# Optimization experiments

Measured on AMD Instinct MI355X. Metric: run time of the kernel, lower is better.

Reference implementation:

```python
import jax, jax.numpy as jnp
import numpy as np
import math

B, T, M, C, H = 2, 2048, 77, 512, 8
D = C // H  # head dim = 64


def setup_inputs() -> dict:
    key = jax.random.key(0)
    ks = jax.random.split(key, 20)
    s = 0.02
    inp = {
        "x": jax.random.normal(ks[0], (B, T, C), jnp.float32),
        "c": jax.random.normal(ks[1], (B, M, C), jnp.float32),
        # causal mask for self-attention (masked_fill where == 0)
        "attn_mask": jnp.tril(jnp.ones((T, T), jnp.int32))[None, None],
        "padding_mask": jnp.ones((B, M), jnp.int32),
    }
    names = ["Wq", "Wk", "Wv", "Wkc", "Wvc", "Wg1", "Wg2", "Wp"]
    for i, n in enumerate(names):
        inp[n] = jax.random.normal(ks[2 + i], (C, C), jnp.float32) * s
        inp["b" + n[1:]] = jnp.zeros((C,), jnp.float32)
    return inp


def _heads(t):
    # [B, S, C] -> [B, S, H, D]
    return t.reshape(t.shape[0], t.shape[1], H, D)


def reference(x, c, attn_mask, padding_mask,
              Wq, bq, Wk, bk, Wv, bv, Wkc, bkc, Wvc, bvc,
              Wg1, bg1, Wg2, bg2, Wp, bp):
    scale = 1.0 / math.sqrt(D)
    q = _heads(x @ Wq + bq)      # [B,T,H,D]
    k = _heads(x @ Wk + bk)      # [B,T,H,D]
    v = _heads(x @ Wv + bv)
    k_c = _heads(c @ Wkc + bkc)  # [B,M,H,D]
    v_c = _heads(c @ Wvc + bvc)

    # self-attention branch
    att = jnp.einsum("bthd,bshd->bhts", q, k) * scale   # [B,H,T,T]
    att = jnp.where(attn_mask == 0, -jnp.inf, att)
    att = jax.nn.softmax(att, axis=-1)
    y = jnp.einsum("bhts,bshd->bthd", att, v).reshape(B, T, C)

    # cross-attention branch to condition c
    att_c = jnp.einsum("bthd,bmhd->bhtm", q, k_c) * scale  # [B,H,T,M]
    att_c = jnp.where(padding_mask[:, None, None, :] == 0, -jnp.inf, att_c)
    att_c = jax.nn.softmax(att_c, axis=-1)
    y_c = jnp.einsum("bhtm,bmhd->bthd", att_c, v_c).reshape(B, T, C)

    # sigmoid gating fusion (note: gates cross-multiply branches, per source)
    gate_self = jax.nn.sigmoid(y @ Wg1 + bg1)
    gate_c = jax.nn.sigmoid(y_c @ Wg2 + bg2)
    y = gate_self * y_c + gate_c * y
    return y @ Wp + bp
```

## Files before the change

kernel.cpp:

```cpp
#include <hip/hip_runtime.h>
#include <hip/hip_bf16.h>
#include <math.h>

#define BB 2
#define TT 2048
#define MM 77
#define CC 512
#define HH 8
#define DD 64

typedef short bf16x8 __attribute__((ext_vector_type(8)));
typedef float f32x4  __attribute__((ext_vector_type(4)));

static __device__ __forceinline__ unsigned short f2bf(float x) {
    __hip_bfloat16 h = __float2bfloat16(x);
    return *reinterpret_cast<unsigned short*>(&h);
}
static __device__ __forceinline__ float bf2f(unsigned short u) {
    unsigned int v = ((unsigned int)u) << 16;
    return *reinterpret_cast<float*>(&v);
}

__global__ __launch_bounds__(256)
void wconv8(const float* __restrict__ w0, const float* __restrict__ w1,
            const float* __restrict__ w2, const float* __restrict__ w3,
            const float* __restrict__ w4, const float* __restrict__ w5,
            const float* __restrict__ w6, const float* __restrict__ w7,
            unsigned short* __restrict__ outbase,
            const float* __restrict__ x, unsigned short* __restrict__ xb)
{
    const float* W;
    switch (blockIdx.z) {
        case 0: W = w0; break; case 1: W = w1; break;
        case 2: W = w2; break; case 3: W = w3; break;
        case 4: W = w4; break; case 5: W = w5; break;
        case 6: W = w6; break; default: W = w7; break;
    }
    unsigned short* Wp = outbase + (size_t)blockIdx.z * 512 * 512;
    const int k0 = blockIdx.x * 64;
    const int n0 = blockIdx.y * 64;
    const int tid = threadIdx.x;
    __shared__ unsigned short t[64 * 72];

    #pragma unroll
    for (int it = 0; it < 4; ++it) {
        const int e = tid + 256 * it;
        const int r  = e >> 4;
        const int c4 = (e & 15) * 4;
        const float4 v = *(const float4*)(W + (size_t)(k0 + r) * 512 + n0 + c4);
        t[(c4 + 0) * 72 + r] = f2bf(v.x);
        t[(c4 + 1) * 72 + r] = f2bf(v.y);
        t[(c4 + 2) * 72 + r] = f2bf(v.z);
        t[(c4 + 3) * 72 + r] = f2bf(v.w);
    }

    {
        const int lin = (blockIdx.z << 6) + (blockIdx.x << 3) + blockIdx.y;
        const size_t base = (size_t)lin * 8 * 512;
        #pragma unroll
        for (int u = 0; u < 2; ++u) {
            const int unit = tid + 256 * u;
            const float4 a = *(const float4*)(x + base + (size_t)unit * 8);
            const float4 b = *(const float4*)(x + base + (size_t)unit * 8 + 4);
            unsigned short o[8];
            o[0] = f2bf(a.x); o[1] = f2bf(a.y); o[2] = f2bf(a.z); o[3] = f2bf(a.w);
            o[4] = f2bf(b.x); o[5] = f2bf(b.y); o[6] = f2bf(b.z); o[7] = f2bf(b.w);
            *(int4*)(xb + base + (size_t)unit * 8) = *(const int4*)o;
        }
    }

    __syncthreads();
    #pragma unroll
    for (int it = 0; it < 2; ++it) {
        const int e    = tid + 256 * it;
        const int gl   = e >> 7;
        const int ktl  = (e >> 6) & 1;
        const int lane = e & 63;
        const int l15  = lane & 15;
        const int q    = lane >> 4;
        const int4 v = *(const int4*)&t[(gl * 16 + l15) * 72 + ktl * 32 + q * 8];
        const int G  = (n0 >> 4) + gl;
        const int KT = (k0 >> 5) + ktl;
        *(int4*)(Wp + ((size_t)(G * 16 + KT) * 64 + lane) * 8) = v;
    }
}

__global__ __launch_bounds__(256)
void proj_all(const unsigned short* __restrict__ xb, const float* __restrict__ cin,
              const unsigned short* __restrict__ Wt8,
              const float* __restrict__ bq, const float* __restrict__ bk,
              const float* __restrict__ bv, const float* __restrict__ bkc,
              const float* __restrict__ bvc,
              unsigned short* __restrict__ qb,
              unsigned short* __restrict__ vtb,
              unsigned short* __restrict__ kcb,
              unsigned short* __restrict__ vtcb)
{
    __shared__ unsigned short As[2 * 16 * 64 * 8];

    const int tid = threadIdx.x;
    int b = blockIdx.x;
    const unsigned short* Wtp;
    const float *bb0, *bb1, *bb2;
    int row0, colb, N, isSelf;
    float oscale;
    if (b < 768) {
        isSelf = 1;
        row0 = (b & 127) * 32; colb = (b >> 7) * 256;
        Wtp = Wt8; N = BB * TT;
        oscale = 0.125f;
        bb0 = bq; bb1 = bk; bb2 = bv;
    } else {
        b -= 768; isSelf = 0;
        row0 = (b % 5) * 32; colb = (b / 5) * 256;
        Wtp = Wt8 + 3 * 262144; N = BB * MM;
        oscale = 1.0f;
        bb0 = bkc; bb1 = bvc; bb2 = nullptr;
    }

    {
        const int r    = tid >> 3;
        const int rg   = r >> 4;
        const int l15r = r & 15;
        const int seg  = (tid & 7) * 64;
        const int gr   = row0 + r;
        unsigned short tmp[64];
        if (isSelf) {
            #pragma unroll
            for (int jb = 0; jb < 8; ++jb)
                *(int4*)&tmp[jb*8] = *(const int4*)(xb + (size_t)gr * 512 + seg + jb * 8);
        } else {
            #pragma unroll
            for (int j = 0; j < 16; ++j) {
                float4 v = (gr < N) ? *(const float4*)(cin + (size_t)gr * 512 + seg + j * 4)
                                    : make_float4(0.f, 0.f, 0.f, 0.f);
                tmp[j*4+0] = f2bf(v.x); tmp[j*4+1] = f2bf(v.y);
                tmp[j*4+2] = f2bf(v.z); tmp[j*4+3] = f2bf(v.w);
            }
        }
        #pragma unroll
        for (int jb = 0; jb < 8; ++jb) {
            const int k  = seg + jb * 8;
            const int kt = k >> 5;
            const int q  = (k >> 3) & 3;
            *(int4*)&As[((rg * 16 + kt) * 64 + q * 16 + l15r) * 8] = *(int4*)&tmp[jb*8];
        }
    }
    __syncthreads();

    const int wv   = tid >> 6;
    const int lane = tid & 63;
    const int l15  = lane & 15;
    const int quad = lane >> 4;
    const int wc   = colb + wv * 64;
    const int wcg  = wc >> 4;

    f32x4 acc[2][4];
    #pragma unroll
    for (int mi = 0; mi < 2; ++mi)
        #pragma unroll
        for (int ni = 0; ni < 4; ++ni) acc[mi][ni] = (f32x4){0.f, 0.f, 0.f, 0.f};

    bf16x8 b0v[4], b1v[4], b2v[4];
    #pragma unroll
    for (int ni = 0; ni < 4; ++ni) {
        b0v[ni] = *(const bf16x8*)(Wtp + (((size_t)(wcg + ni) * 16 + 0) << 9) + lane * 8);
        b1v[ni] = *(const bf16x8*)(Wtp + (((size_t)(wcg + ni) * 16 + 1) << 9) + lane * 8);
    }

    for (int kt = 0; kt < 16; ++kt) {
        if (kt + 2 < 16) {
            #pragma unroll
            for (int ni = 0; ni < 4; ++ni)
                b2v[ni] = *(const bf16x8*)(Wtp + (((size_t)(wcg + ni) * 16 + kt + 2) << 9) + lane * 8);
        }
        const bf16x8 a0 = *(const bf16x8*)&As[((0 * 16 + kt) * 64 + lane) * 8];
        const bf16x8 a1 = *(const bf16x8*)&As[((1 * 16 + kt) * 64 + lane) * 8];
        #pragma unroll
        for (int ni = 0; ni < 4; ++ni) {
            acc[0][ni] = __builtin_amdgcn_mfma_f32_16x16x32_bf16(a0, b0v[ni], acc[0][ni], 0, 0, 0);
            acc[1][ni] = __builtin_amdgcn_mfma_f32_16x16x32_bf16(a1, b0v[ni], acc[1][ni], 0, 0, 0);
        }
        #pragma unroll
        for (int ni = 0; ni < 4; ++ni) { b0v[ni] = b1v[ni]; b1v[ni] = b2v[ni]; }
    }

    const int which = wc >> 9;
    const float* bsel = (which == 0) ? bb0 : ((which == 1) ? bb1 : bb2);
    const float sc = (which == 0) ? oscale : 1.f;

    float bvv[4];
    #pragma unroll
    for (int ni = 0; ni < 4; ++ni)
        bvv[ni] = bsel[(wc + ni * 16 + l15) & 511];

    if (isSelf) {
        const int b_ = row0 >> 11;
        const int t0 = row0 & 2047;
        const int h  = (wc & 511) >> 6;
        __syncthreads();
        if (which < 2) {
            unsigned short* TL = (unsigned short*)As + wv * (32 * 72);
            #pragma unroll
            for (int mi = 0; mi < 2; ++mi)
                #pragma unroll
                for (int ni = 0; ni < 4; ++ni)
                    #pragma unroll
                    for (int reg = 0; reg < 4; ++reg) {
                        const int t = mi * 16 + quad * 4 + reg;
                        const int d = ni * 16 + l15;
                        TL[t * 72 + d] = f2bf((acc[mi][ni][reg] + bvv[ni]) * sc);
                    }
            unsigned short* dst = qb + (size_t)which * 2097152
                                + (((size_t)b_ * 8 + h) * 2048 + t0) * 64;
            #pragma unroll
            for (int it = 0; it < 4; ++it) {
                const int t = it * 8 + (lane >> 3);
                *(int4*)(dst + (size_t)t * 64 + (lane & 7) * 8)
                    = *(const int4*)&TL[t * 72 + (lane & 7) * 8];
            }
        } else {
            unsigned short* TL = (unsigned short*)As + wv * (64 * 40);
            #pragma unroll
            for (int mi = 0; mi < 2; ++mi)
                #pragma unroll
                for (int ni = 0; ni < 4; ++ni) {
                    ushort4 u;
                    u.x = f2bf(acc[mi][ni][0] + bvv[ni]);
                    u.y = f2bf(acc[mi][ni][1] + bvv[ni]);
                    u.z = f2bf(acc[mi][ni][2] + bvv[ni]);
                    u.w = f2bf(acc[mi][ni][3] + bvv[ni]);
                    const int d = ni * 16 + l15;
                    *(ushort4*)&TL[d * 40 + mi * 16 + quad * 4] = u;
                }
            unsigned short* dst = vtb + (((size_t)b_ * 8 + h) * 64) * 2048 + t0;
            #pragma unroll
            for (int it = 0; it < 4; ++it) {
                const int d = it * 16 + (lane >> 2);
                *(int4*)(dst + (size_t)d * 2048 + (lane & 3) * 8)
                    = *(const int4*)&TL[d * 40 + (lane & 3) * 8];
            }
        }
    } else {
        #pragma unroll
        for (int mi = 0; mi < 2; ++mi)
            #pragma unroll
            for (int reg = 0; reg < 4; ++reg) {
                const int row = row0 + mi * 16 + quad * 4 + reg;
                if (row >= N) continue;
                const int b_ = (row >= MM) ? 1 : 0;
                const int m_ = row - b_ * MM;
                #pragma unroll
                for (int ni = 0; ni < 4; ++ni) {
                    const float v = acc[mi][ni][reg] + bvv[ni];
                    const int cl = (wc + ni * 16 + l15) & 511;
                    const int hh = cl >> 6, d = cl & 63;
                    if (which == 0)
                        kcb[(((size_t)b_ * 8 + hh) * 77 + m_) * 64 + d] = f2bf(v);
                    else
                        vtcb[(((size_t)b_ * 8 + hh) * 64 + d) * 128 + m_] = f2bf(v);
                }
            }
        if (which == 1 && row0 == 0) {
            const int h0 = (colb - 512) >> 6;
            for (int e = tid; e < 2 * 4 * 64; e += 256) {
                const int d  = e & 63;
                const int hl = (e >> 6) & 3;
                const int bz = e >> 8;
                unsigned short* rp = vtcb + (((size_t)bz * 8 + h0 + hl) * 64 + d) * 128;
                rp[77] = 0; rp[78] = 0; rp[79] = 0;
                #pragma unroll
                for (int q8 = 80; q8 < 128; q8 += 8)
                    *(int4*)(rp + q8) = make_int4(0, 0, 0, 0);
            }
        }
    }
}

__global__ __launch_bounds__(256)
void attn_all(const unsigned short* __restrict__ Qh,
              const unsigned short* __restrict__ Kh,
              const unsigned short* __restrict__ Vth,
              unsigned short* __restrict__ yout,
              const unsigned short* __restrict__ Kch,
              const unsigned short* __restrict__ Vtch,
              unsigned short* __restrict__ ycout)
{
    int lin = blockIdx.x;
    int causal, S_kv, W, bh, qt;
    const unsigned short *Kb, *Vb;
    unsigned short* outp;
    if (lin < 512) {
        causal = 1; S_kv = TT; W = TT;
        bh = (lin & 7) | (((lin >> 3) & 1) << 3);
        const int qtr = lin >> 4;
        qt = (qtr < 16) ? (31 - qtr) : (qtr - 16);
        Kb = Kh + (size_t)bh * S_kv * 64;
        Vb = Vth + (size_t)bh * 64 * W;
        outp = yout;
    } else {
        lin -= 512;
        causal = 0; S_kv = MM; W = 128;
        bh = (lin & 7) | (((lin >> 3) & 1) << 3);
        qt = lin >> 4;
        Kb = Kch + (size_t)bh * S_kv * 64;
        Vb = Vtch + (size_t)bh * 64 * W;
        outp = ycout;
    }
    const int n_kt = causal ? (qt + 1) : 2;

    const int tid  = threadIdx.x;
    const int wv   = tid >> 6;
    const int lane = tid & 63;
    const int l15  = lane & 15;
    const int quad = lane >> 4;

    __shared__ unsigned short Ks[64 * 80];
    __shared__ unsigned short Vs[64 * 80];
    __shared__ unsigned short PT[4 * 16 * 72];

    const int t0 = qt * 64 + wv * 16;
    const unsigned short* qptr = Qh + ((size_t)bh * TT + t0 + l15) * 64 + quad * 8;
    const bf16x8 qb0 = *(const bf16x8*)(qptr);
    const bf16x8 qb1 = *(const bf16x8*)(qptr + 32);

    f32x4 Oacc[4];
    #pragma unroll
    for (int dt = 0; dt < 4; ++dt) Oacc[dt] = (f32x4){0.f, 0.f, 0.f, 0.f};
    float l = 0.f;

    int4 kR[2], vR[2];
    {
        #pragma unroll
        for (int it = 0; it < 2; ++it) {
            const int e = tid + 256 * it;
            const int row = e >> 3, blk = e & 7;
            kR[it] = (row < S_kv)
                ? *(const int4*)(Kb + (size_t)row * 64 + blk * 8) : make_int4(0,0,0,0);
            vR[it] = (blk * 8 < W)
                ? *(const int4*)(Vb + (size_t)row * W + blk * 8) : make_int4(0,0,0,0);
        }
        #pragma unroll
        for (int it = 0; it < 2; ++it) {
            const int e = tid + 256 * it;
            const int row = e >> 3, blk = e & 7;
            *(int4*)&Ks[row * 80 + ((blk ^ (row & 7)) * 8)] = kR[it];
            *(int4*)&Vs[row * 80 + ((blk ^ (row & 7)) * 8)] = vR[it];
        }
    }
    __syncthreads();

    for (int kt = 0; kt < n_kt; ++kt) {
        const int s0 = kt * 64;

        if (kt + 1 < n_kt) {
            const int s1 = (kt + 1) * 64;
            #pragma unroll
            for (int it = 0; it < 2; ++it) {
                const int e = tid + 256 * it;
                const int row = e >> 3, blk = e & 7;
                const int s = s1 + row;
                kR[it] = (s < S_kv)
                    ? *(const int4*)(Kb + (size_t)s * 64 + blk * 8) : make_int4(0,0,0,0);
                vR[it] = (s1 + blk * 8 < W)
                    ? *(const int4*)(Vb + (size_t)row * W + s1 + blk * 8) : make_int4(0,0,0,0);
            }
        }

        f32x4 sacc[4];
        __builtin_amdgcn_s_setprio(1);
        #pragma unroll
        for (int mt = 0; mt < 4; ++mt) {
            const int krow = 16 * mt + l15;
            const bf16x8 ka0 = *(const bf16x8*)&Ks[krow * 80 + (((quad    ) ^ (krow & 7)) * 8)];
            const bf16x8 ka1 = *(const bf16x8*)&Ks[krow * 80 + (((quad + 4) ^ (krow & 7)) * 8)];
            sacc[mt] = (f32x4){0.f, 0.f, 0.f, 0.f};
            sacc[mt] = __builtin_amdgcn_mfma_f32_16x16x32_bf16(ka0, qb0, sacc[mt], 0, 0, 0);
            sacc[mt] = __builtin_amdgcn_mfma_f32_16x16x32_bf16(ka1, qb1, sacc[mt], 0, 0, 0);
        }
        __builtin_amdgcn_s_setprio(0);

        float sv[16];
        #pragma unroll
        for (int mt = 0; mt < 4; ++mt)
            #pragma unroll
            for (int reg = 0; reg < 4; ++reg)
                sv[mt * 4 + reg] = sacc[mt][reg];

        const bool cmask = (causal && kt == qt);
        if (cmask || (s0 + 64 > S_kv)) {
            const int lim = cmask ? (t0 + l15) : 0x7fffffff;
            #pragma unroll
            for (int mt = 0; mt < 4; ++mt)
                #pragma unroll
                for (int reg = 0; reg < 4; ++reg) {
                    const int kg = s0 + 16 * mt + quad * 4 + reg;
                    if (kg > lim || kg >= S_kv) sv[mt * 4 + reg] = -INFINITY;
                }
        }

        float p[16], psum = 0.f;
        #pragma unroll
        for (int i = 0; i < 16; ++i) { p[i] = __expf(sv[i]); psum += p[i]; }
        psum += __shfl_xor(psum, 16);
        psum += __shfl_xor(psum, 32);
        l += psum;

        unsigned short* ptw = &PT[wv * 16 * 72 + l15 * 72];
        #pragma unroll
        for (int mt = 0; mt < 4; ++mt) {
            ushort4 u;
            u.x = f2bf(p[mt * 4 + 0]); u.y = f2bf(p[mt * 4 + 1]);
            u.z = f2bf(p[mt * 4 + 2]); u.w = f2bf(p[mt * 4 + 3]);
            *(ushort4*)(ptw + 16 * mt + quad * 4) = u;
        }
        const bf16x8 pb0 = *(const bf16x8*)(ptw + quad * 8);
        const bf16x8 pb1 = *(const bf16x8*)(ptw + quad * 8 + 32);

        __builtin_amdgcn_s_setprio(1);
        #pragma unroll
        for (int dt = 0; dt < 4; ++dt) {
            const int vrow = 16 * dt + l15;
            const bf16x8 va0 = *(const bf16x8*)&Vs[vrow * 80 + (((quad    ) ^ (vrow & 7)) * 8)];
            const bf16x8 va1 = *(const bf16x8*)&Vs[vrow * 80 + (((quad + 4) ^ (vrow & 7)) * 8)];
            Oacc[dt] = __builtin_amdgcn_mfma_f32_16x16x32_bf16(va0, pb0, Oacc[dt], 0, 0, 0);
            Oacc[dt] = __builtin_amdgcn_mfma_f32_16x16x32_bf16(va1, pb1, Oacc[dt], 0, 0, 0);
        }
        __builtin_amdgcn_s_setprio(0);

        if (kt + 1 < n_kt) {
            __syncthreads();
            #pragma unroll
            for (int it = 0; it < 2; ++it) {
                const int e = tid + 256 * it;
                const int row = e >> 3, blk = e & 7;
                *(int4*)&Ks[row * 80 + ((blk ^ (row & 7)) * 8)] = kR[it];
                *(int4*)&Vs[row * 80 + ((blk ^ (row & 7)) * 8)] = vR[it];
            }
            __syncthreads();
        }
    }

    const int b = bh >> 3, h = bh & 7;
    const float inv_l = 1.f / l;
    const int t = t0 + l15;
    unsigned short* ob = outp + ((size_t)b * TT + t) * CC + h * DD + quad * 4;
    #pragma unroll
    for (int dt = 0; dt < 4; ++dt) {
        ushort4 u;
        u.x = f2bf(Oacc[dt][0] * inv_l);
        u.y = f2bf(Oacc[dt][1] * inv_l);
        u.z = f2bf(Oacc[dt][2] * inv_l);
        u.w = f2bf(Oacc[dt][3] * inv_l);
        *(ushort4*)(ob + 16 * dt) = u;
    }
}

__global__ __launch_bounds__(512)
void gates_final(const unsigned short* __restrict__ yb,
                 const unsigned short* __restrict__ ycb,
                 const unsigned short* __restrict__ Wt8,
                 const float* __restrict__ bg1, const float* __restrict__ bg2,
                 const float* __restrict__ bp,
                 float* __restrict__ out)
{
    __shared__ unsigned short Ay[16 * 512];
    __shared__ unsigned short Ac[16 * 512];

    const int tid  = threadIdx.x;
    const int row0 = blockIdx.x * 16;

    {
        const int r  = tid >> 5;
        const int c0 = (tid & 31) * 16;
        const unsigned short* ys = yb  + (size_t)(row0 + r) * 512 + c0;
        const unsigned short* cs = ycb + (size_t)(row0 + r) * 512 + c0;
        #pragma unroll
        for (int jb = 0; jb < 2; ++jb) {
            const int k  = c0 + jb * 8;
            const int kt = k >> 5;
            const int q  = (k >> 3) & 3;
            *(int4*)&Ay[(kt * 64 + q * 16 + r) * 8] = *(const int4*)(ys + jb * 8);
            *(int4*)&Ac[(kt * 64 + q * 16 + r) * 8] = *(const int4*)(cs + jb * 8);
        }
    }
    __syncthreads();

    const int wv   = tid >> 6;
    const int lane = tid & 63;
    const int l15  = lane & 15;
    const int quad = lane >> 4;
    const int wc   = wv * 64;
    const int wcg  = wc >> 4;

    const unsigned short* W1 = Wt8 + 5 * 262144;
    const unsigned short* W2 = Wt8 + 6 * 262144;
    const unsigned short* W3 = Wt8 + 7 * 262144;

    unsigned int g1p[8], g2p[8];

    #pragma unroll
    for (int gg = 0; gg < 2; ++gg) {
        const unsigned short* Wg = gg ? W2 : W1;
        const unsigned short* Ax = gg ? Ac : Ay;
        const float* bg = gg ? bg2 : bg1;
        f32x4 acc[4];
        #pragma unroll
        for (int ni = 0; ni < 4; ++ni) acc[ni] = (f32x4){0.f, 0.f, 0.f, 0.f};
        bf16x8 b0v[4], b1v[4], b2v[4];
        #pragma unroll
        for (int ni = 0; ni < 4; ++ni) {
            b0v[ni] = *(const bf16x8*)(Wg + (((size_t)(wcg + ni) * 16 + 0) << 9) + lane * 8);
            b1v[ni] = *(const bf16x8*)(Wg + (((size_t)(wcg + ni) * 16 + 1) << 9) + lane * 8);
        }
        for (int kt = 0; kt < 16; ++kt) {
            if (kt + 2 < 16) {
                #pragma unroll
                for (int ni = 0; ni < 4; ++ni)
                    b2v[ni] = *(const bf16x8*)(Wg + (((size_t)(wcg + ni) * 16 + kt + 2) << 9) + lane * 8);
            }
            const bf16x8 a = *(const bf16x8*)&Ax[(kt * 64 + lane) * 8];
            #pragma unroll
            for (int ni = 0; ni < 4; ++ni)
                acc[ni] = __builtin_amdgcn_mfma_f32_16x16x32_bf16(a, b0v[ni], acc[ni], 0, 0, 0);
            #pragma unroll
            for (int ni = 0; ni < 4; ++ni) { b0v[ni] = b1v[ni]; b1v[ni] = b2v[ni]; }
        }
        #pragma unroll
        for (int ni = 0; ni < 4; ++ni) {
            const float bv = bg[wc + ni * 16 + l15];
            float s[4];
            #pragma unroll
            for (int reg = 0; reg < 4; ++reg) {
                const float v = acc[ni][reg] + bv;
                s[reg] = 1.f / (1.f + __expf(-v));
            }
            const unsigned int p01 = (unsigned int)f2bf(s[0]) | ((unsigned int)f2bf(s[1]) << 16);
            const unsigned int p23 = (unsigned int)f2bf(s[2]) | ((unsigned int)f2bf(s[3]) << 16);
            if (gg == 0) {
                g1p[ni * 2 + 0] = p01;
                g1p[ni * 2 + 1] = p23;
            } else {
                g2p[ni * 2 + 0] = p01;
                g2p[ni * 2 + 1] = p23;
            }
        }
    }

    unsigned short zp[16];
    #pragma unroll
    for (int ni = 0; ni < 4; ++ni) {
        #pragma unroll
        for (int reg = 0; reg < 4; ++reg) {
            const int r = quad * 4 + reg;
            const int c = wc + ni * 16 + l15;
            const int addr = ((c >> 5) * 64 + ((c >> 3) & 3) * 16 + r) * 8 + (c & 7);
            const float yv = bf2f(Ay[addr]);
            const float cv = bf2f(Ac[addr]);
            const unsigned int p1 = g1p[ni * 2 + (reg >> 1)];
            const unsigned int p2 = g2p[ni * 2 + (reg >> 1)];
            const unsigned short g1v = (reg & 1) ? (unsigned short)(p1 >> 16) : (unsigned short)(p1 & 0xffff);
            const unsigned short g2v = (reg & 1) ? (unsigned short)(p2 >> 16) : (unsigned short)(p2 & 0xffff);
            zp[ni * 4 + reg] = f2bf(bf2f(g1v) * cv + bf2f(g2v) * yv);
        }
    }
    __syncthreads();
    #pragma unroll
    for (int ni = 0; ni < 4; ++ni)
        #pragma unroll
        for (int reg = 0; reg < 4; ++reg) {
            const int r = quad * 4 + reg;
            const int c = wc + ni * 16 + l15;
            Ay[((c >> 5) * 64 + ((c >> 3) & 3) * 16 + r) * 8 + (c & 7)] = zp[ni * 4 + reg];
        }
    __syncthreads();

    {
        f32x4 acc[4];
        #pragma unroll
        for (int ni = 0; ni < 4; ++ni) acc[ni] = (f32x4){0.f, 0.f, 0.f, 0.f};
        bf16x8 b0v[4], b1v[4], b2v[4];
        #pragma unroll
        for (int ni = 0; ni < 4; ++ni) {
            b0v[ni] = *(const bf16x8*)(W3 + (((size_t)(wcg + ni) * 16 + 0) << 9) + lane * 8);
            b1v[ni] = *(const bf16x8*)(W3 + (((size_t)(wcg + ni) * 16 + 1) << 9) + lane * 8);
        }
        for (int kt = 0; kt < 16; ++kt) {
            if (kt + 2 < 16) {
                #pragma unroll
                for (int ni = 0; ni < 4; ++ni)
                    b2v[ni] = *(const bf16x8*)(W3 + (((size_t)(wcg + ni) * 16 + kt + 2) << 9) + lane * 8);
            }
            const bf16x8 a = *(const bf16x8*)&Ay[(kt * 64 + lane) * 8];
            #pragma unroll
            for (int ni = 0; ni < 4; ++ni)
                acc[ni] = __builtin_amdgcn_mfma_f32_16x16x32_bf16(a, b0v[ni], acc[ni], 0, 0, 0);
            #pragma unroll
            for (int ni = 0; ni < 4; ++ni) { b0v[ni] = b1v[ni]; b1v[ni] = b2v[ni]; }
        }
        #pragma unroll
        for (int ni = 0; ni < 4; ++ni) {
            const int col = wc + ni * 16 + l15;
            const float bv = bp[col];
            #pragma unroll
            for (int reg = 0; reg < 4; ++reg) {
                const int row = row0 + quad * 4 + reg;
                out[(size_t)row * 512 + col] = acc[ni][reg] + bv;
            }
        }
    }
}

extern "C" void kernel_launch(void* const* d_in, const int* in_sizes, int n_in,
                              void* d_out, int out_size, void* d_ws, size_t ws_size,
                              hipStream_t stream)
{
    const float* x   = (const float*)d_in[0];
    const float* cin = (const float*)d_in[1];
    const float* Wq  = (const float*)d_in[4];   const float* bq  = (const float*)d_in[5];
    const float* Wk  = (const float*)d_in[6];   const float* bk  = (const float*)d_in[7];
    const float* Wv  = (const float*)d_in[8];   const float* bv  = (const float*)d_in[9];
    const float* Wkc = (const float*)d_in[10];  const float* bkc = (const float*)d_in[11];
    const float* Wvc = (const float*)d_in[12];  const float* bvc = (const float*)d_in[13];
    const float* Wg1 = (const float*)d_in[14];  const float* bg1 = (const float*)d_in[15];
    const float* Wg2 = (const float*)d_in[16];  const float* bg2 = (const float*)d_in[17];
    const float* Wp  = (const float*)d_in[18];  const float* bp  = (const float*)d_in[19];

    float* out = (float*)d_out;
    char*  w   = (char*)d_ws;
    const size_t MB = 1024 * 1024;

    unsigned short* Wt8  = (unsigned short*)(w);
    unsigned short* qb   = (unsigned short*)(w + 4  * MB);
    unsigned short* vtb  = (unsigned short*)(w + 16 * MB);
    unsigned short* yb   = (unsigned short*)(w + 20 * MB);
    unsigned short* ycb  = (unsigned short*)(w + 24 * MB);
    unsigned short* xb   = (unsigned short*)(w + 28 * MB);
    unsigned short* kcb  = (unsigned short*)(w + 40 * MB);
    unsigned short* vtcb = (unsigned short*)(w + 40 * MB + 512 * 1024);

    const dim3 blk(256);

    wconv8<<<dim3(8, 8, 8), blk, 0, stream>>>(Wq, Wk, Wv, Wkc, Wvc, Wg1, Wg2, Wp,
                                              Wt8, x, xb);

    proj_all<<<dim3(788), blk, 0, stream>>>(
        xb, cin, Wt8, bq, bk, bv, bkc, bvc, qb, vtb, kcb, vtcb);

    attn_all<<<dim3(1024), blk, 0, stream>>>(
        qb, qb + 2097152, vtb, yb, kcb, vtcb, ycb);

    gates_final<<<dim3(256), dim3(512), 0, stream>>>(
        yb, ycb, Wt8, bg1, bg2, bp, out);
}
```

Before: 192.8 us.

## Pair complementary causal query tiles per block to share K/V loads

```diff
diff --git a/kernel.cpp b/kernel.cpp
--- a/kernel.cpp
+++ b/kernel.cpp
@@ -287,27 +287,30 @@
               unsigned short* __restrict__ ycout)
 {
     int lin = blockIdx.x;
-    int causal, S_kv, W, bh, qt;
+    int causal, S_kv, W, bh, q0t, q1t, hasQ1, n_kt;
     const unsigned short *Kb, *Vb;
     unsigned short* outp;
-    if (lin < 512) {
+    if (lin < 256) {
         causal = 1; S_kv = TT; W = TT;
         bh = (lin & 7) | (((lin >> 3) & 1) << 3);
-        const int qtr = lin >> 4;
-        qt = (qtr < 16) ? (31 - qtr) : (qtr - 16);
+        const int j = lin >> 4;
+        q0t = 31 - j;
+        q1t = j;
+        hasQ1 = 1;
+        n_kt = 32 - j;
         Kb = Kh + (size_t)bh * S_kv * 64;
         Vb = Vth + (size_t)bh * 64 * W;
         outp = yout;
     } else {
-        lin -= 512;
+        lin -= 256;
         causal = 0; S_kv = MM; W = 128;
         bh = (lin & 7) | (((lin >> 3) & 1) << 3);
-        qt = lin >> 4;
+        q0t = lin >> 4; q1t = 0; hasQ1 = 0;
+        n_kt = 2;
         Kb = Kch + (size_t)bh * S_kv * 64;
         Vb = Vtch + (size_t)bh * 64 * W;
         outp = ycout;
     }
-    const int n_kt = causal ? (qt + 1) : 2;
 
     const int tid  = threadIdx.x;
     const int wv   = tid >> 6;
@@ -317,17 +320,24 @@
 
     __shared__ unsigned short Ks[64 * 80];
     __shared__ unsigned short Vs[64 * 80];
-    __shared__ unsigned short PT[4 * 16 * 72];
-
-    const int t0 = qt * 64 + wv * 16;
-    const unsigned short* qptr = Qh + ((size_t)bh * TT + t0 + l15) * 64 + quad * 8;
-    const bf16x8 qb0 = *(const bf16x8*)(qptr);
-    const bf16x8 qb1 = *(const bf16x8*)(qptr + 32);
-
-    f32x4 Oacc[4];
-    #pragma unroll
-    for (int dt = 0; dt < 4; ++dt) Oacc[dt] = (f32x4){0.f, 0.f, 0.f, 0.f};
-    float l = 0.f;
+    __shared__ unsigned short PT[2][4 * 16 * 72];
+
+    const int t0 = q0t * 64 + wv * 16;
+    const int t1 = q1t * 64 + wv * 16;
+    const unsigned short* qp0 = Qh + ((size_t)bh * TT + t0 + l15) * 64 + quad * 8;
+    const bf16x8 q00 = *(const bf16x8*)(qp0);
+    const bf16x8 q01 = *(const bf16x8*)(qp0 + 32);
+    const unsigned short* qp1 = Qh + ((size_t)bh * TT + t1 + l15) * 64 + quad * 8;
+    const bf16x8 q10 = *(const bf16x8*)(qp1);
+    const bf16x8 q11 = *(const bf16x8*)(qp1 + 32);
+
+    f32x4 O0[4], O1[4];
+    #pragma unroll
+    for (int dt = 0; dt < 4; ++dt) {
+        O0[dt] = (f32x4){0.f, 0.f, 0.f, 0.f};
+        O1[dt] = (f32x4){0.f, 0.f, 0.f, 0.f};
+    }
+    float l0 = 0.f, l1 = 0.f;
 
     int4 kR[2], vR[2];
     {
@@ -367,55 +377,102 @@
             }
         }
 
-        f32x4 sacc[4];
+        const int a1 = hasQ1 && (kt <= q1t);
+
+        f32x4 sacc0[4], sacc1[4];
         __builtin_amdgcn_s_setprio(1);
         #pragma unroll
         for (int mt = 0; mt < 4; ++mt) {
             const int krow = 16 * mt + l15;
             const bf16x8 ka0 = *(const bf16x8*)&Ks[krow * 80 + (((quad    ) ^ (krow & 7)) * 8)];
             const bf16x8 ka1 = *(const bf16x8*)&Ks[krow * 80 + (((quad + 4) ^ (krow & 7)) * 8)];
-            sacc[mt] = (f32x4){0.f, 0.f, 0.f, 0.f};
-            sacc[mt] = __builtin_amdgcn_mfma_f32_16x16x32_bf16(ka0, qb0, sacc[mt], 0, 0, 0);
-            sacc[mt] = __builtin_amdgcn_mfma_f32_16x16x32_bf16(ka1, qb1, sacc[mt], 0, 0, 0);
+            sacc0[mt] = (f32x4){0.f, 0.f, 0.f, 0.f};
+            sacc0[mt] = __builtin_amdgcn_mfma_f32_16x16x32_bf16(ka0, q00, sacc0[mt], 0, 0, 0);
+            sacc0[mt] = __builtin_amdgcn_mfma_f32_16x16x32_bf16(ka1, q01, sacc0[mt], 0, 0, 0);
+            if (a1) {
+                sacc1[mt] = (f32x4){0.f, 0.f, 0.f, 0.f};
+                sacc1[mt] = __builtin_amdgcn_mfma_f32_16x16x32_bf16(ka0, q10, sacc1[mt], 0, 0, 0);
+                sacc1[mt] = __builtin_amdgcn_mfma_f32_16x16x32_bf16(ka1, q11, sacc1[mt], 0, 0, 0);
+            }
         }
         __builtin_amdgcn_s_setprio(0);
 
-        float sv[16];
-        #pragma unroll
-        for (int mt = 0; mt < 4; ++mt)
-            #pragma unroll
-            for (int reg = 0; reg < 4; ++reg)
-                sv[mt * 4 + reg] = sacc[mt][reg];
-
-        const bool cmask = (causal && kt == qt);
-        if (cmask || (s0 + 64 > S_kv)) {
-            const int lim = cmask ? (t0 + l15) : 0x7fffffff;
+        {
+            float sv[16];
             #pragma unroll
             for (int mt = 0; mt < 4; ++mt)
                 #pragma unroll
-                for (int reg = 0; reg < 4; ++reg) {
-                    const int kg = s0 + 16 * mt + quad * 4 + reg;
-                    if (kg > lim || kg >= S_kv) sv[mt * 4 + reg] = -INFINITY;
-                }
-        }
-
-        float p[16], psum = 0.f;
-        #pragma unroll
-        for (int i = 0; i < 16; ++i) { p[i] = __expf(sv[i]); psum += p[i]; }
-        psum += __shfl_xor(psum, 16);
-        psum += __shfl_xor(psum, 32);
-        l += psum;
-
-        unsigned short* ptw = &PT[wv * 16 * 72 + l15 * 72];
-        #pragma unroll
-        for (int mt = 0; mt < 4; ++mt) {
-            ushort4 u;
-            u.x = f2bf(p[mt * 4 + 0]); u.y = f2bf(p[mt * 4 + 1]);
-            u.z = f2bf(p[mt * 4 + 2]); u.w = f2bf(p[mt * 4 + 3]);
-            *(ushort4*)(ptw + 16 * mt + quad * 4) = u;
-        }
-        const bf16x8 pb0 = *(const bf16x8*)(ptw + quad * 8);
-        const bf16x8 pb1 = *(const bf16x8*)(ptw + quad * 8 + 32);
+                for (int reg = 0; reg < 4; ++reg)
+                    sv[mt * 4 + reg] = sacc0[mt][reg];
+            const bool cmask = (causal && kt == q0t);
+            if (cmask || (s0 + 64 > S_kv)) {
+                const int lim = cmask ? (t0 + l15) : 0x7fffffff;
+                #pragma unroll
+                for (int mt = 0; mt < 4; ++mt)
+                    #pragma unroll
+                    for (int reg = 0; reg < 4; ++reg) {
+                        const int kg = s0 + 16 * mt + quad * 4 + reg;
+                        if (kg > lim || kg >= S_kv) sv[mt * 4 + reg] = -INFINITY;
+                    }
+            }
+            float p[16], psum = 0.f;
+            #pragma unroll
+            for (int i = 0; i < 16; ++i) { p[i] = __expf(sv[i]); psum += p[i]; }
+            psum += __shfl_xor(psum, 16);
+            psum += __shfl_xor(psum, 32);
+            l0 += psum;
+            unsigned short* ptw = &PT[0][wv * 16 * 72 + l15 * 72];
+            #pragma unroll
+            for (int mt = 0; mt < 4; ++mt) {
+                ushort4 u;
+                u.x = f2bf(p[mt * 4 + 0]); u.y = f2bf(p[mt * 4 + 1]);
+                u.z = f2bf(p[mt * 4 + 2]); u.w = f2bf(p[mt * 4 + 3]);
+                *(ushort4*)(ptw + 16 * mt + quad * 4) = u;
+            }
+        }
+
+        if (a1) {
+            float sv[16];
+            #pragma unroll
+            for (int mt = 0; mt < 4; ++mt)
+                #pragma unroll
+                for (int reg = 0; reg < 4; ++reg)
+                    sv[mt * 4 + reg] = sacc1[mt][reg];
+            if (kt == q1t) {
+                const int lim = t1 + l15;
+                #pragma unroll
+                for (int mt = 0; mt < 4; ++mt)
+                    #pragma unroll
+                    for (int reg = 0; reg < 4; ++reg) {
+                        const int kg = s0 + 16 * mt + quad * 4 + reg;
+                        if (kg > lim) sv[mt * 4 + reg] = -INFINITY;
+                    }
+            }
+            float p[16], psum = 0.f;
+            #pragma unroll
+            for (int i = 0; i < 16; ++i) { p[i] = __expf(sv[i]); psum += p[i]; }
+            psum += __shfl_xor(psum, 16);
+            psum += __shfl_xor(psum, 32);
+            l1 += psum;
+            unsigned short* ptw = &PT[1][wv * 16 * 72 + l15 * 72];
+            #pragma unroll
+            for (int mt = 0; mt < 4; ++mt) {
+                ushort4 u;
+                u.x = f2bf(p[mt * 4 + 0]); u.y = f2bf(p[mt * 4 + 1]);
+                u.z = f2bf(p[mt * 4 + 2]); u.w = f2bf(p[mt * 4 + 3]);
+                *(ushort4*)(ptw + 16 * mt + quad * 4) = u;
+            }
+        }
+
+        const unsigned short* ptr0 = &PT[0][wv * 16 * 72 + l15 * 72];
+        const bf16x8 pb00 = *(const bf16x8*)(ptr0 + quad * 8);
+        const bf16x8 pb01 = *(const bf16x8*)(ptr0 + quad * 8 + 32);
+        bf16x8 pb10, pb11;
+        if (a1) {
+            const unsigned short* ptr1 = &PT[1][wv * 16 * 72 + l15 * 72];
+            pb10 = *(const bf16x8*)(ptr1 + quad * 8);
+            pb11 = *(const bf16x8*)(ptr1 + quad * 8 + 32);
+        }
 
         __builtin_amdgcn_s_setprio(1);
         #pragma unroll
@@ -423,8 +480,12 @@
             const int vrow = 16 * dt + l15;
             const bf16x8 va0 = *(const bf16x8*)&Vs[vrow * 80 + (((quad    ) ^ (vrow & 7)) * 8)];
             const bf16x8 va1 = *(const bf16x8*)&Vs[vrow * 80 + (((quad + 4) ^ (vrow & 7)) * 8)];
-            Oacc[dt] = __builtin_amdgcn_mfma_f32_16x16x32_bf16(va0, pb0, Oacc[dt], 0, 0, 0);
-            Oacc[dt] = __builtin_amdgcn_mfma_f32_16x16x32_bf16(va1, pb1, Oacc[dt], 0, 0, 0);
+            O0[dt] = __builtin_amdgcn_mfma_f32_16x16x32_bf16(va0, pb00, O0[dt], 0, 0, 0);
+            O0[dt] = __builtin_amdgcn_mfma_f32_16x16x32_bf16(va1, pb01, O0[dt], 0, 0, 0);
+            if (a1) {
+                O1[dt] = __builtin_amdgcn_mfma_f32_16x16x32_bf16(va0, pb10, O1[dt], 0, 0, 0);
+                O1[dt] = __builtin_amdgcn_mfma_f32_16x16x32_bf16(va1, pb11, O1[dt], 0, 0, 0);
+            }
         }
         __builtin_amdgcn_s_setprio(0);
 
@@ -442,17 +503,33 @@
     }
 
     const int b = bh >> 3, h = bh & 7;
-    const float inv_l = 1.f / l;
-    const int t = t0 + l15;
-    unsigned short* ob = outp + ((size_t)b * TT + t) * CC + h * DD + quad * 4;
-    #pragma unroll
-    for (int dt = 0; dt < 4; ++dt) {
-        ushort4 u;
-        u.x = f2bf(Oacc[dt][0] * inv_l);
-        u.y = f2bf(Oacc[dt][1] * inv_l);
-        u.z = f2bf(Oacc[dt][2] * inv_l);
-        u.w = f2bf(Oacc[dt][3] * inv_l);
-        *(ushort4*)(ob + 16 * dt) = u;
+    {
+        const float inv_l = 1.f / l0;
+        const int t = t0 + l15;
+        unsigned short* ob = outp + ((size_t)b * TT + t) * CC + h * DD + quad * 4;
+        #pragma unroll
+        for (int dt = 0; dt < 4; ++dt) {
+            ushort4 u;
+            u.x = f2bf(O0[dt][0] * inv_l);
+            u.y = f2bf(O0[dt][1] * inv_l);
+            u.z = f2bf(O0[dt][2] * inv_l);
+            u.w = f2bf(O0[dt][3] * inv_l);
+            *(ushort4*)(ob + 16 * dt) = u;
+        }
+    }
+    if (hasQ1) {
+        const float inv_l = 1.f / l1;
+        const int t = t1 + l15;
+        unsigned short* ob = outp + ((size_t)b * TT + t) * CC + h * DD + quad * 4;
+        #pragma unroll
+        for (int dt = 0; dt < 4; ++dt) {
+            ushort4 u;
+            u.x = f2bf(O1[dt][0] * inv_l);
+            u.y = f2bf(O1[dt][1] * inv_l);
+            u.z = f2bf(O1[dt][2] * inv_l);
+            u.w = f2bf(O1[dt][3] * inv_l);
+            *(ushort4*)(ob + 16 * dt) = u;
+        }
     }
 }
 
@@ -647,7 +724,7 @@
     proj_all<<<dim3(788), blk, 0, stream>>>(
         xb, cin, Wt8, bq, bk, bv, bkc, bvc, qb, vtb, kcb, vtcb);
 
-    attn_all<<<dim3(1024), blk, 0, stream>>>(
+    attn_all<<<dim3(768), blk, 0, stream>>>(
         qb, qb + 2097152, vtb, yb, kcb, vtcb, ycb);
 
     gates_final<<<dim3(256), dim3(512), 0, stream>>>(
```

After: 197.5 us. 2.4% more time.

## Split causal attention KV range into two halves with fp32 partial merge in gating kernel

Applied to the files above, without the earlier changes.

```diff
diff --git a/kernel.cpp b/kernel.cpp
--- a/kernel.cpp
+++ b/kernel.cpp
@@ -281,33 +281,35 @@
 void attn_all(const unsigned short* __restrict__ Qh,
               const unsigned short* __restrict__ Kh,
               const unsigned short* __restrict__ Vth,
-              unsigned short* __restrict__ yout,
+              float* __restrict__ part0, float* __restrict__ part1,
+              float* __restrict__ lp,
               const unsigned short* __restrict__ Kch,
               const unsigned short* __restrict__ Vtch,
               unsigned short* __restrict__ ycout)
 {
     int lin = blockIdx.x;
-    int causal, S_kv, W, bh, qt;
+    int causal, S_kv, W, bh, qt, ktb, kte, half;
     const unsigned short *Kb, *Vb;
-    unsigned short* outp;
-    if (lin < 512) {
+    if (lin < 1024) {
         causal = 1; S_kv = TT; W = TT;
         bh = (lin & 7) | (((lin >> 3) & 1) << 3);
-        const int qtr = lin >> 4;
+        const int rest = lin >> 4;
+        half = rest & 1;
+        const int qtr = rest >> 1;
         qt = (qtr < 16) ? (31 - qtr) : (qtr - 16);
+        const int h0 = (qt + 2) >> 1;
+        ktb = half ? h0 : 0;
+        kte = half ? (qt + 1) : h0;
         Kb = Kh + (size_t)bh * S_kv * 64;
         Vb = Vth + (size_t)bh * 64 * W;
-        outp = yout;
     } else {
-        lin -= 512;
+        lin -= 1024;
         causal = 0; S_kv = MM; W = 128;
         bh = (lin & 7) | (((lin >> 3) & 1) << 3);
-        qt = lin >> 4;
+        qt = lin >> 4; ktb = 0; kte = 2; half = 0;
         Kb = Kch + (size_t)bh * S_kv * 64;
         Vb = Vtch + (size_t)bh * 64 * W;
-        outp = ycout;
-    }
-    const int n_kt = causal ? (qt + 1) : 2;
+    }
 
     const int tid  = threadIdx.x;
     const int wv   = tid >> 6;
@@ -329,107 +331,19 @@
     for (int dt = 0; dt < 4; ++dt) Oacc[dt] = (f32x4){0.f, 0.f, 0.f, 0.f};
     float l = 0.f;
 
-    int4 kR[2], vR[2];
-    {
-        #pragma unroll
-        for (int it = 0; it < 2; ++it) {
-            const int e = tid + 256 * it;
-            const int row = e >> 3, blk = e & 7;
-            kR[it] = (row < S_kv)
-                ? *(const int4*)(Kb + (size_t)row * 64 + blk * 8) : make_int4(0,0,0,0);
-            vR[it] = (blk * 8 < W)
-                ? *(const int4*)(Vb + (size_t)row * W + blk * 8) : make_int4(0,0,0,0);
-        }
-        #pragma unroll
-        for (int it = 0; it < 2; ++it) {
-            const int e = tid + 256 * it;
-            const int row = e >> 3, blk = e & 7;
-            *(int4*)&Ks[row * 80 + ((blk ^ (row & 7)) * 8)] = kR[it];
-            *(int4*)&Vs[row * 80 + ((blk ^ (row & 7)) * 8)] = vR[it];
-        }
-    }
-    __syncthreads();
-
-    for (int kt = 0; kt < n_kt; ++kt) {
-        const int s0 = kt * 64;
-
-        if (kt + 1 < n_kt) {
-            const int s1 = (kt + 1) * 64;
+    if (ktb < kte) {
+        int4 kR[2], vR[2];
+        {
+            const int sbase = ktb * 64;
             #pragma unroll
             for (int it = 0; it < 2; ++it) {
                 const int e = tid + 256 * it;
                 const int row = e >> 3, blk = e & 7;
-                const int s = s1 + row;
-                kR[it] = (s < S_kv)
-                    ? *(const int4*)(Kb + (size_t)s * 64 + blk * 8) : make_int4(0,0,0,0);
-                vR[it] = (s1 + blk * 8 < W)
-                    ? *(const int4*)(Vb + (size_t)row * W + s1 + blk * 8) : make_int4(0,0,0,0);
-            }
-        }
-
-        f32x4 sacc[4];
-        __builtin_amdgcn_s_setprio(1);
-        #pragma unroll
-        for (int mt = 0; mt < 4; ++mt) {
-            const int krow = 16 * mt + l15;
-            const bf16x8 ka0 = *(const bf16x8*)&Ks[krow * 80 + (((quad    ) ^ (krow & 7)) * 8)];
-            const bf16x8 ka1 = *(const bf16x8*)&Ks[krow * 80 + (((quad + 4) ^ (krow & 7)) * 8)];
-            sacc[mt] = (f32x4){0.f, 0.f, 0.f, 0.f};
-            sacc[mt] = __builtin_amdgcn_mfma_f32_16x16x32_bf16(ka0, qb0, sacc[mt], 0, 0, 0);
-            sacc[mt] = __builtin_amdgcn_mfma_f32_16x16x32_bf16(ka1, qb1, sacc[mt], 0, 0, 0);
-        }
-        __builtin_amdgcn_s_setprio(0);
-
-        float sv[16];
-        #pragma unroll
-        for (int mt = 0; mt < 4; ++mt)
-            #pragma unroll
-            for (int reg = 0; reg < 4; ++reg)
-                sv[mt * 4 + reg] = sacc[mt][reg];
-
-        const bool cmask = (causal && kt == qt);
-        if (cmask || (s0 + 64 > S_kv)) {
-            const int lim = cmask ? (t0 + l15) : 0x7fffffff;
-            #pragma unroll
-            for (int mt = 0; mt < 4; ++mt)
-                #pragma unroll
-                for (int reg = 0; reg < 4; ++reg) {
-                    const int kg = s0 + 16 * mt + quad * 4 + reg;
-                    if (kg > lim || kg >= S_kv) sv[mt * 4 + reg] = -INFINITY;
-                }
-        }
-
-        float p[16], psum = 0.f;
-        #pragma unroll
-        for (int i = 0; i < 16; ++i) { p[i] = __expf(sv[i]); psum += p[i]; }
-        psum += __shfl_xor(psum, 16);
-        psum += __shfl_xor(psum, 32);
-        l += psum;
-
-        unsigned short* ptw = &PT[wv * 16 * 72 + l15 * 72];
-        #pragma unroll
-        for (int mt = 0; mt < 4; ++mt) {
-            ushort4 u;
-            u.x = f2bf(p[mt * 4 + 0]); u.y = f2bf(p[mt * 4 + 1]);
-            u.z = f2bf(p[mt * 4 + 2]); u.w = f2bf(p[mt * 4 + 3]);
-            *(ushort4*)(ptw + 16 * mt + quad * 4) = u;
-        }
-        const bf16x8 pb0 = *(const bf16x8*)(ptw + quad * 8);
-        const bf16x8 pb1 = *(const bf16x8*)(ptw + quad * 8 + 32);
-
-        __builtin_amdgcn_s_setprio(1);
-        #pragma unroll
-        for (int dt = 0; dt < 4; ++dt) {
-            const int vrow = 16 * dt + l15;
-            const bf16x8 va0 = *(const bf16x8*)&Vs[vrow * 80 + (((quad    ) ^ (vrow & 7)) * 8)];
-            const bf16x8 va1 = *(const bf16x8*)&Vs[vrow * 80 + (((quad + 4) ^ (vrow & 7)) * 8)];
-            Oacc[dt] = __builtin_amdgcn_mfma_f32_16x16x32_bf16(va0, pb0, Oacc[dt], 0, 0, 0);
-            Oacc[dt] = __builtin_amdgcn_mfma_f32_16x16x32_bf16(va1, pb1, Oacc[dt], 0, 0, 0);
-        }
-        __builtin_amdgcn_s_setprio(0);
-
-        if (kt + 1 < n_kt) {
-            __syncthreads();
+                kR[it] = (sbase + row < S_kv)
+                    ? *(const int4*)(Kb + (size_t)(sbase + row) * 64 + blk * 8) : make_int4(0,0,0,0);
+                vR[it] = (sbase + blk * 8 < W)
+                    ? *(const int4*)(Vb + (size_t)row * W + sbase + blk * 8) : make_int4(0,0,0,0);
+            }
             #pragma unroll
             for (int it = 0; it < 2; ++it) {
                 const int e = tid + 256 * it;
@@ -437,27 +351,129 @@
                 *(int4*)&Ks[row * 80 + ((blk ^ (row & 7)) * 8)] = kR[it];
                 *(int4*)&Vs[row * 80 + ((blk ^ (row & 7)) * 8)] = vR[it];
             }
-            __syncthreads();
+        }
+        __syncthreads();
+
+        for (int kt = ktb; kt < kte; ++kt) {
+            const int s0 = kt * 64;
+
+            if (kt + 1 < kte) {
+                const int s1 = (kt + 1) * 64;
+                #pragma unroll
+                for (int it = 0; it < 2; ++it) {
+                    const int e = tid + 256 * it;
+                    const int row = e >> 3, blk = e & 7;
+                    const int s = s1 + row;
+                    kR[it] = (s < S_kv)
+                        ? *(const int4*)(Kb + (size_t)s * 64 + blk * 8) : make_int4(0,0,0,0);
+                    vR[it] = (s1 + blk * 8 < W)
+                        ? *(const int4*)(Vb + (size_t)row * W + s1 + blk * 8) : make_int4(0,0,0,0);
+                }
+            }
+
+            f32x4 sacc[4];
+            __builtin_amdgcn_s_setprio(1);
+            #pragma unroll
+            for (int mt = 0; mt < 4; ++mt) {
+                const int krow = 16 * mt + l15;
+                const bf16x8 ka0 = *(const bf16x8*)&Ks[krow * 80 + (((quad    ) ^ (krow & 7)) * 8)];
+                const bf16x8 ka1 = *(const bf16x8*)&Ks[krow * 80 + (((quad + 4) ^ (krow & 7)) * 8)];
+                sacc[mt] = (f32x4){0.f, 0.f, 0.f, 0.f};
+                sacc[mt] = __builtin_amdgcn_mfma_f32_16x16x32_bf16(ka0, qb0, sacc[mt], 0, 0, 0);
+                sacc[mt] = __builtin_amdgcn_mfma_f32_16x16x32_bf16(ka1, qb1, sacc[mt], 0, 0, 0);
+            }
+            __builtin_amdgcn_s_setprio(0);
+
+            float sv[16];
+            #pragma unroll
+            for (int mt = 0; mt < 4; ++mt)
+                #pragma unroll
+                for (int reg = 0; reg < 4; ++reg)
+                    sv[mt * 4 + reg] = sacc[mt][reg];
+
+            const bool cmask = (causal && kt == qt);
+            if (cmask || (s0 + 64 > S_kv)) {
+                const int lim = cmask ? (t0 + l15) : 0x7fffffff;
+                #pragma unroll
+                for (int mt = 0; mt < 4; ++mt)
+                    #pragma unroll
+                    for (int reg = 0; reg < 4; ++reg) {
+                        const int kg = s0 + 16 * mt + quad * 4 + reg;
+                        if (kg > lim || kg >= S_kv) sv[mt * 4 + reg] = -INFINITY;
+                    }
+            }
+
+            float p[16], psum = 0.f;
+            #pragma unroll
+            for (int i = 0; i < 16; ++i) { p[i] = __expf(sv[i]); psum += p[i]; }
+            psum += __shfl_xor(psum, 16);
+            psum += __shfl_xor(psum, 32);
+            l += psum;
+
+            unsigned short* ptw = &PT[wv * 16 * 72 + l15 * 72];
+            #pragma unroll
+            for (int mt = 0; mt < 4; ++mt) {
+                ushort4 u;
+                u.x = f2bf(p[mt * 4 + 0]); u.y = f2bf(p[mt * 4 + 1]);
+                u.z = f2bf(p[mt * 4 + 2]); u.w = f2bf(p[mt * 4 + 3]);
+                *(ushort4*)(ptw + 16 * mt + quad * 4) = u;
+            }
+            const bf16x8 pb0 = *(const bf16x8*)(ptw + quad * 8);
+            const bf16x8 pb1 = *(const bf16x8*)(ptw + quad * 8 + 32);
+
+            __builtin_amdgcn_s_setprio(1);
+            #pragma unroll
+            for (int dt = 0; dt < 4; ++dt) {
+                const int vrow = 16 * dt + l15;
+                const bf16x8 va0 = *(const bf16x8*)&Vs[vrow * 80 + (((quad    ) ^ (vrow & 7)) * 8)];
+                const bf16x8 va1 = *(const bf16x8*)&Vs[vrow * 80 + (((quad + 4) ^ (vrow & 7)) * 8)];
+                Oacc[dt] = __builtin_amdgcn_mfma_f32_16x16x32_bf16(va0, pb0, Oacc[dt], 0, 0, 0);
+                Oacc[dt] = __builtin_amdgcn_mfma_f32_16x16x32_bf16(va1, pb1, Oacc[dt], 0, 0, 0);
+            }
+            __builtin_amdgcn_s_setprio(0);
+
+            if (kt + 1 < kte) {
+                __syncthreads();
+                #pragma unroll
+                for (int it = 0; it < 2; ++it) {
+                    const int e = tid + 256 * it;
+                    const int row = e >> 3, blk = e & 7;
+                    *(int4*)&Ks[row * 80 + ((blk ^ (row & 7)) * 8)] = kR[it];
+                    *(int4*)&Vs[row * 80 + ((blk ^ (row & 7)) * 8)] = vR[it];
+                }
+                __syncthreads();
+            }
         }
     }
 
     const int b = bh >> 3, h = bh & 7;
-    const float inv_l = 1.f / l;
-    const int t = t0 + l15;
-    unsigned short* ob = outp + ((size_t)b * TT + t) * CC + h * DD + quad * 4;
-    #pragma unroll
-    for (int dt = 0; dt < 4; ++dt) {
-        ushort4 u;
-        u.x = f2bf(Oacc[dt][0] * inv_l);
-        u.y = f2bf(Oacc[dt][1] * inv_l);
-        u.z = f2bf(Oacc[dt][2] * inv_l);
-        u.w = f2bf(Oacc[dt][3] * inv_l);
-        *(ushort4*)(ob + 16 * dt) = u;
+    if (causal) {
+        float* sel = half ? part1 : part0;
+        float* pO = sel + ((size_t)(b * TT + t0 + l15) * CC) + h * DD + quad * 4;
+        #pragma unroll
+        for (int dt = 0; dt < 4; ++dt)
+            *(f32x4*)(pO + 16 * dt) = Oacc[dt];
+        if (quad == 0)
+            lp[(((size_t)half * 2 + b) * 8 + h) * 2048 + t0 + l15] = l;
+    } else {
+        const float inv_l = 1.f / l;
+        const int t = t0 + l15;
+        unsigned short* ob = ycout + ((size_t)b * TT + t) * CC + h * DD + quad * 4;
+        #pragma unroll
+        for (int dt = 0; dt < 4; ++dt) {
+            ushort4 u;
+            u.x = f2bf(Oacc[dt][0] * inv_l);
+            u.y = f2bf(Oacc[dt][1] * inv_l);
+            u.z = f2bf(Oacc[dt][2] * inv_l);
+            u.w = f2bf(Oacc[dt][3] * inv_l);
+            *(ushort4*)(ob + 16 * dt) = u;
+        }
     }
 }
 
 __global__ __launch_bounds__(512)
-void gates_final(const unsigned short* __restrict__ yb,
+void gates_final(const float* __restrict__ part0, const float* __restrict__ part1,
+                 const float* __restrict__ lp,
                  const unsigned short* __restrict__ ycb,
                  const unsigned short* __restrict__ Wt8,
                  const float* __restrict__ bg1, const float* __restrict__ bg2,
@@ -473,16 +489,27 @@
     {
         const int r  = tid >> 5;
         const int c0 = (tid & 31) * 16;
-        const unsigned short* ys = yb  + (size_t)(row0 + r) * 512 + c0;
-        const unsigned short* cs = ycb + (size_t)(row0 + r) * 512 + c0;
-        #pragma unroll
-        for (int jb = 0; jb < 2; ++jb) {
-            const int k  = c0 + jb * 8;
-            const int kt = k >> 5;
-            const int q  = (k >> 3) & 3;
-            *(int4*)&Ay[(kt * 64 + q * 16 + r) * 8] = *(const int4*)(ys + jb * 8);
-            *(int4*)&Ac[(kt * 64 + q * 16 + r) * 8] = *(const int4*)(cs + jb * 8);
-        }
+        const int row = row0 + r;
+        const int b = row >> 11;
+        const int t = row & 2047;
+        const int h = c0 >> 6;
+        const float la = lp[(((size_t)0 * 2 + b) * 8 + h) * 2048 + t];
+        const float lb = lp[(((size_t)1 * 2 + b) * 8 + h) * 2048 + t];
+        const float inv_l = 1.f / (la + lb);
+        const float* pa = part0 + (size_t)row * 512 + c0;
+        const float* pb = part1 + (size_t)row * 512 + c0;
+        unsigned short yv[16];
+        #pragma unroll
+        for (int j = 0; j < 16; ++j)
+            yv[j] = f2bf((pa[j] + pb[j]) * inv_l);
+
+        const unsigned short* cs = ycb + (size_t)row * 512 + c0;
+        const int kt = c0 >> 5;
+        const int q  = (c0 >> 3) & 3;
+        *(int4*)&Ay[(kt * 64 + (q + 0) * 16 + r) * 8] = *(const int4*)&yv[0];
+        *(int4*)&Ay[(kt * 64 + (q + 1) * 16 + r) * 8] = *(const int4*)&yv[8];
+        *(int4*)&Ac[(kt * 64 + (q + 0) * 16 + r) * 8] = *(const int4*)(cs + 0);
+        *(int4*)&Ac[(kt * 64 + (q + 1) * 16 + r) * 8] = *(const int4*)(cs + 8);
     }
     __syncthreads();
 
@@ -630,14 +657,16 @@
     char*  w   = (char*)d_ws;
     const size_t MB = 1024 * 1024;
 
-    unsigned short* Wt8  = (unsigned short*)(w);
-    unsigned short* qb   = (unsigned short*)(w + 4  * MB);
-    unsigned short* vtb  = (unsigned short*)(w + 16 * MB);
-    unsigned short* yb   = (unsigned short*)(w + 20 * MB);
-    unsigned short* ycb  = (unsigned short*)(w + 24 * MB);
-    unsigned short* xb   = (unsigned short*)(w + 28 * MB);
-    unsigned short* kcb  = (unsigned short*)(w + 40 * MB);
-    unsigned short* vtcb = (unsigned short*)(w + 40 * MB + 512 * 1024);
+    unsigned short* Wt8   = (unsigned short*)(w);
+    unsigned short* qb    = (unsigned short*)(w + 4  * MB);
+    unsigned short* vtb   = (unsigned short*)(w + 12 * MB);
+    unsigned short* ycb   = (unsigned short*)(w + 16 * MB);
+    unsigned short* xb    = (unsigned short*)(w + 20 * MB);
+    float*          part0 = (float*)(w + 24 * MB);
+    float*          part1 = (float*)(w + 32 * MB);
+    float*          lp    = (float*)(w + 40 * MB);
+    unsigned short* kcb   = (unsigned short*)(w + 41 * MB);
+    unsigned short* vtcb  = (unsigned short*)(w + 41 * MB + 256 * 1024);
 
     const dim3 blk(256);
 
@@ -647,9 +676,9 @@
     proj_all<<<dim3(788), blk, 0, stream>>>(
         xb, cin, Wt8, bq, bk, bv, bkc, bvc, qb, vtb, kcb, vtcb);
 
-    attn_all<<<dim3(1024), blk, 0, stream>>>(
-        qb, qb + 2097152, vtb, yb, kcb, vtcb, ycb);
+    attn_all<<<dim3(1536), blk, 0, stream>>>(
+        qb, qb + 2097152, vtb, part0, part1, lp, kcb, vtcb, ycb);
 
     gates_final<<<dim3(256), dim3(512), 0, stream>>>(
-        yb, ycb, Wt8, bg1, bg2, bp, out);
+        part0, part1, lp, ycb, Wt8, bg1, bg2, bp, out);
 }
```

After: 180.9 us. 6.2% less time.
